# Kernel tuning notes

Hardware: AMD Instinct MI355X
Metric: run time of the kernel (lower is better)

The kernel has to match this reference:

```python
import jax, jax.numpy as jnp
import numpy as np

TOPOLOGY = [0,0,1,2,3,4,0,6,7,8,0,10,11,12,12,14,15,16,12,18,19,20]
J = len(TOPOLOGY)          # 22 joints
POS, OFF = 3, 1            # position_feature, offset_feature
CIN = (POS + OFF) * J      # 88 conv channels


def _adj():
    # adj[parent, child] = 1 (root skipped), fixed skeleton adjacency
    a = np.zeros((J, J), np.float32)
    for i, p in enumerate(TOPOLOGY):
        if i:
            a[p, i] = 1.0
    return jnp.asarray(a)


def setup_inputs() -> dict:
    key = jax.random.key(0)
    ks = jax.random.split(key, 32)

    def n(k, shape, s):
        return jax.random.normal(k, shape, dtype=jnp.float32) * s

    inp = {
        "input": jax.random.normal(ks[0], (128, 2048, J, POS), dtype=jnp.float32),
        "offset": jax.random.normal(ks[1], (128, 2048, J, OFF), dtype=jnp.float32),
    }
    i = 2
    for c in ("conv1", "conv2", "conv3"):
        inp[c + "_w"] = n(ks[i], (CIN, CIN, 4), 0.05); i += 1  # OIH
        inp[c + "_b"] = jnp.zeros((CIN,), jnp.float32)
    for g in ("g1", "g2"):
        inp[g + "_n2n_w"] = n(ks[i], (POS, POS), 0.3); i += 1
        inp[g + "_n2n_b"] = jnp.zeros((POS,), jnp.float32)
        inp[g + "_e2n_we"] = n(ks[i], (OFF, POS), 0.3); i += 1
        inp[g + "_e2n_wn"] = n(ks[i], (POS, POS), 0.3); i += 1
        inp[g + "_e2n_b"] = jnp.zeros((POS,), jnp.float32)
        inp[g + "_n2e_wn"] = n(ks[i], (POS, OFF), 0.3); i += 1
        inp[g + "_n2e_we"] = n(ks[i], (OFF, OFF), 0.3); i += 1
        inp[g + "_n2e_b"] = jnp.zeros((OFF,), jnp.float32)
        inp[g + "_lin_w"] = n(ks[i], (2 * POS, POS), 0.3); i += 1
        inp[g + "_lin_b"] = jnp.zeros((POS,), jnp.float32)
    return inp


def _conv_block(x, off, w, b):
    # concat node+edge feats, fold (joint, feature) into channels, temporal Conv1d k=4 s=2 p=1
    x = jnp.concatenate([x, off], axis=-1)          # [B,F,J,C]
    B, F, Jn, C = x.shape
    y = x.transpose(0, 2, 3, 1).reshape(B, Jn * C, F)
    y = jax.lax.conv_general_dilated(y, w, window_strides=(2,), padding=[(1, 1)],
                                     dimension_numbers=("NCH", "OIH", "NCH"))
    y = y + b[None, :, None]
    Fn = y.shape[-1]                                # F // 2
    return y.transpose(0, 2, 1).reshape(B, Fn, Jn, C)


def _graph_block(x, A, n2n_w, n2n_b, e2n_we, e2n_wn, e2n_b,
                 n2e_wn, n2e_we, n2e_b, lin_w, lin_b):
    node, edge = x[..., :POS], x[..., POS:]
    # adjacency broadcast (torch code replicated it B*F times; same math)
    agg_n = jnp.einsum('ij,bfjc->bfic', A, node)
    agg_e = jnp.einsum('ij,bfjc->bfic', A, edge)
    f1 = agg_n @ n2n_w + n2n_b                              # Node2Node
    f2 = agg_e @ e2n_we + node @ e2n_wn + e2n_b             # Edge2Node
    new_edge = jnp.einsum('ji,bfjc->bfic', A, node) @ n2e_wn + edge @ n2e_we + n2e_b  # Node2Edge
    h = jnp.concatenate([f1, f2], axis=-1) @ lin_w + lin_b  # fuse 2*c_out_node -> c_out_node
    return h, new_edge


def reference(input, offset,
              conv1_w, conv1_b, conv2_w, conv2_b, conv3_w, conv3_b,
              g1_n2n_w, g1_n2n_b, g1_e2n_we, g1_e2n_wn, g1_e2n_b,
              g1_n2e_wn, g1_n2e_we, g1_n2e_b, g1_lin_w, g1_lin_b,
              g2_n2n_w, g2_n2n_b, g2_e2n_we, g2_e2n_wn, g2_e2n_b,
              g2_n2e_wn, g2_n2e_we, g2_n2e_b, g2_lin_w, g2_lin_b):
    A = _adj()
    x = _conv_block(input, offset, conv1_w, conv1_b)
    x, off = _graph_block(x, A, g1_n2n_w, g1_n2n_b, g1_e2n_we, g1_e2n_wn, g1_e2n_b,
                          g1_n2e_wn, g1_n2e_we, g1_n2e_b, g1_lin_w, g1_lin_b)
    x = _conv_block(x, off, conv2_w, conv2_b)
    x, off = _graph_block(x, A, g2_n2n_w, g2_n2n_b, g2_e2n_we, g2_e2n_wn, g2_e2n_b,
                          g2_n2e_wn, g2_n2e_we, g2_n2e_b, g2_lin_w, g2_lin_b)
    x = _conv_block(x, off, conv3_w, conv3_b)
    return x[..., :POS]   # final slice when last dim != c_out_node
```

## Files before the change

kernel.cpp:

```cpp
#include <hip/hip_runtime.h>


static constexpr int Jn   = 22;
static constexpr int C4   = 88;
static constexpr int KK   = 352;
static constexpr int NPAD = 96;
static constexpr int LROW = 88;
static constexpr int YROW = 101;
static constexpr int WSWZ = 2 * 11 * 3 * 64 * 8;

typedef __attribute__((ext_vector_type(8))) short    short8;
typedef __attribute__((ext_vector_type(4))) float    floatx4;
typedef __attribute__((ext_vector_type(4))) unsigned uintx4;

__device__ constexpr int TOPc[Jn] = {0,0,1,2,3,4,0,6,7,8,0,10,11,12,12,14,15,16,12,18,19,20};

__device__ __forceinline__ unsigned short f2bf(float f) {
    unsigned u = __builtin_bit_cast(unsigned, f);
    unsigned r = (u + 0x7FFFu + ((u >> 16) & 1u)) >> 16;
    return (unsigned short)r;
}
__device__ __forceinline__ int qmap(int q) {
    return (q < 66) ? 4 * (q / 3) + (q % 3) : 4 * (q - 66) + 3;
}

struct GW {
    const float *n2n_w, *n2n_b, *e2n_we, *e2n_wn, *e2n_b;
    const float *n2e_wn, *n2e_we, *n2e_b, *lin_w, *lin_b;
};

__global__ __launch_bounds__(256)
void prep_weights(const float* __restrict__ w1, const float* __restrict__ w2,
                  const float* __restrict__ w3,
                  const float* __restrict__ b1, const float* __restrict__ b2,
                  const float* __restrict__ b3,
                  unsigned short* __restrict__ wo, float* __restrict__ bo)
{
    const int i = blockIdx.x * 256 + threadIdx.x;
    if (i < 3 * WSWZ) {
        const int s = i / WSWZ, e = i - s * WSWZ;
        const int j = e & 7, t = e >> 3;
        const int lane = t & 63, t2 = t >> 6;
        const int nti = t2 % 3, t3 = t2 / 3;
        const int kt = t3 % 11, nh = t3 / 11;
        const int co = nh * 48 + nti * 16 + (lane & 15);
        const int k  = kt * 32 + 8 * (lane >> 4) + j;
        const int tap = k / C4, q = k - tap * C4;
        const float* w = (s == 0) ? w1 : (s == 1) ? w2 : w3;
        float v = 0.f;
        if (co < C4) v = w[((size_t)qmap(co) * C4 + qmap(q)) * 4 + tap];
        wo[i] = f2bf(v);
    } else if (i < 3 * WSWZ + 3 * NPAD) {
        const int jj = i - 3 * WSWZ;
        const int s = jj / NPAD, q = jj - s * NPAD;
        const float* bb = (s == 0) ? b1 : (s == 1) ? b2 : b3;
        bo[jj] = (q < C4) ? bb[qmap(q)] : 0.f;
    }
}

template<int FIN, int INM, int OUTM, int MTt>
__global__ __launch_bounds__(256, (MTt == 128 ? 2 : 4))
void conv_fused(const float* __restrict__ xf, const float* __restrict__ xoff,
                const unsigned short* __restrict__ xbf,
                const unsigned short* __restrict__ bwz, const float* __restrict__ bias,
                void* __restrict__ yout, GW g)
{
    constexpr int FOUT  = FIN / 2;
    constexpr int NTILE = FOUT / MTt;
    constexpr int NFRt  = 2 * MTt + 2;
    constexpr int NMT   = MTt / 32;
    constexpr int CHK_N  = NFRt * 11;
    constexpr int NIT_C  = (CHK_N + 255) / 256;
    constexpr int NGRP   = 256 / MTt;
    constexpr int JPG    = (Jn + NGRP - 1) / NGRP;
    constexpr unsigned XBYTES = NFRt * LROW * 2;
    constexpr unsigned SMEM = (OUTM == 0)
        ? (MTt * YROW * 4 + MTt * C4 * 2)
        : (XBYTES + MTt * 66 * 4);

    __shared__ __align__(16) unsigned char smem[SMEM];
    unsigned short* Xs = reinterpret_cast<unsigned short*>(smem);
    float*          Yt = reinterpret_cast<float*>(smem);
    unsigned short* OutU = reinterpret_cast<unsigned short*>(smem + (size_t)MTt * YROW * 4);
    float*          OutF = reinterpret_cast<float*>(smem + XBYTES);

    const int tid = threadIdx.x;
    const int b   = blockIdx.x / NTILE;
    const int fo0 = (blockIdx.x - b * NTILE) * MTt;
    const int gf0 = 2 * fo0 - 1;

    if (INM == 0) {
        const float* nbase = xf   + (size_t)b * FIN * 66;
        const float* ebase = xoff + (size_t)b * FIN * 22;
#pragma unroll
        for (int it = 0; it < NIT_C; ++it) {
            const int idx = tid + it * 256;
            if (idx < CHK_N) {
                const int lf = idx / 11, qq = idx - lf * 11;
                const int gf = gf0 + lf;
                const int gfc = min(max(gf, 0), FIN - 1);
                const float* nrow = nbase + (size_t)gfc * 66;
                const float* erow = ebase + (size_t)gfc * 22;
                uintx4 u;
#pragma unroll
                for (int k = 0; k < 4; ++k) {
                    const int gq = qq * 8 + 2 * k;
                    const float* src = (gq >= 66) ? (erow + (gq - 66)) : (nrow + gq);
                    const float2 v = *reinterpret_cast<const float2*>(src);
                    u[k] = (unsigned)f2bf(v.x) | ((unsigned)f2bf(v.y) << 16);
                }
                if (gf != gfc) u = (uintx4){0u, 0u, 0u, 0u};
                *reinterpret_cast<uintx4*>(Xs + lf * LROW + qq * 8) = u;
            }
        }
    } else {
        const uintx4* xsrc = reinterpret_cast<const uintx4*>(xbf) + (size_t)b * FIN * 11;
#pragma unroll
        for (int it = 0; it < NIT_C; ++it) {
            const int idx = tid + it * 256;
            if (idx < CHK_N) {
                const int lf = idx / 11, qq = idx - lf * 11;
                const int gf = gf0 + lf;
                const int gfc = min(max(gf, 0), FIN - 1);
                uintx4 v = xsrc[gfc * 11 + qq];
                if (gf != gfc) v = (uintx4){0u, 0u, 0u, 0u};
                *reinterpret_cast<uintx4*>(Xs + lf * LROW + qq * 8) = v;
            }
        }
    }
    __syncthreads();

    const int wid = tid >> 6, lane = tid & 63;
    const int l15 = lane & 15, h = lane >> 4;
    const int mhalf = wid >> 1, nhalf = wid & 1;

    floatx4 acc[NMT][3];
#pragma unroll
    for (int mt = 0; mt < NMT; ++mt)
#pragma unroll
        for (int nti = 0; nti < 3; ++nti)
            acc[mt][nti] = (floatx4){0.f, 0.f, 0.f, 0.f};

    const unsigned short* wb = bwz + ((size_t)nhalf * 33 * 64 + lane) * 8;

#pragma unroll
    for (int kt = 0; kt < 11; ++kt) {
        const int q   = 4 * kt + h;
        const int tap = (unsigned)q / 11u;
        const int ci0 = 8 * (q - 11 * tap);
        const int lfb = 2 * l15 + tap;

        short8 afr[NMT];
#pragma unroll
        for (int mt = 0; mt < NMT; ++mt)
            afr[mt] = *reinterpret_cast<const short8*>(
                Xs + (mhalf * MTt + mt * 32 + lfb) * LROW + ci0);

        short8 bfr[3];
#pragma unroll
        for (int nti = 0; nti < 3; ++nti)
            bfr[nti] = *reinterpret_cast<const short8*>(wb + (size_t)(kt * 3 + nti) * 64 * 8);

#pragma unroll
        for (int mt = 0; mt < NMT; ++mt)
#pragma unroll
            for (int nti = 0; nti < 3; ++nti)
                acc[mt][nti] = __builtin_amdgcn_mfma_f32_16x16x32_bf16(
                    afr[mt], bfr[nti], acc[mt][nti], 0, 0, 0);
    }

    if (OUTM == 1) {
#pragma unroll
        for (int mt = 0; mt < NMT; ++mt)
#pragma unroll
            for (int nti = 0; nti < 3; ++nti) {
                const int co = nhalf * 48 + nti * 16 + l15;
                if (co < 66) {
                    const float bi = bias[co];
#pragma unroll
                    for (int r = 0; r < 4; ++r) {
                        const int row = mhalf * (MTt / 2) + mt * 16 + 4 * h + r;
                        OutF[row * 66 + co] = acc[mt][nti][r] + bi;
                    }
                }
            }
        __syncthreads();
        float2* dstg = reinterpret_cast<float2*>(
            reinterpret_cast<float*>(yout) + (size_t)(b * FOUT + fo0) * 66);
        const float2* srcl = reinterpret_cast<const float2*>(OutF);
        constexpr int NOUT2 = MTt * 33;
#pragma unroll
        for (int it = 0; it < (NOUT2 + 255) / 256; ++it) {
            const int idx = tid + it * 256;
            if (idx < NOUT2) dstg[idx] = srcl[idx];
        }
        return;
    }

    __syncthreads();
#pragma unroll
    for (int mt = 0; mt < NMT; ++mt)
#pragma unroll
        for (int nti = 0; nti < 3; ++nti) {
            const int co = nhalf * 48 + nti * 16 + l15;
            const float bi = bias[co];
#pragma unroll
            for (int r = 0; r < 4; ++r) {
                const int row = mhalf * (MTt / 2) + mt * 16 + 4 * h + r;
                Yt[row * YROW + co] = acc[mt][nti][r] + bi;
            }
        }
    __syncthreads();

    {
        const int row = tid & (MTt - 1), grp = tid / MTt;
        const float* yr = Yt + row * YROW;

        float n2n[9], n2nb[3], e2we[3], e2wn[9], e2nb[3], newn[3], lin[18], linb[3];
#pragma unroll
        for (int i = 0; i < 9;  ++i) n2n[i]  = g.n2n_w[i];
#pragma unroll
        for (int i = 0; i < 3;  ++i) n2nb[i] = g.n2n_b[i];
#pragma unroll
        for (int i = 0; i < 3;  ++i) e2we[i] = g.e2n_we[i];
#pragma unroll
        for (int i = 0; i < 9;  ++i) e2wn[i] = g.e2n_wn[i];
#pragma unroll
        for (int i = 0; i < 3;  ++i) e2nb[i] = g.e2n_b[i];
#pragma unroll
        for (int i = 0; i < 3;  ++i) newn[i] = g.n2e_wn[i];
        const float newe = g.n2e_we[0];
        const float neb  = g.n2e_b[0];
#pragma unroll
        for (int i = 0; i < 18; ++i) lin[i]  = g.lin_w[i];
#pragma unroll
        for (int i = 0; i < 3;  ++i) linb[i] = g.lin_b[i];

#pragma unroll
        for (int i = 0; i < Jn; ++i) {
            if (i / JPG != grp) continue;
            float an0 = 0.f, an1 = 0.f, an2 = 0.f, ae = 0.f;
#pragma unroll
            for (int j = 1; j < Jn; ++j) {
                if (TOPc[j] == i) {
                    an0 += yr[3 * j]; an1 += yr[3 * j + 1];
                    an2 += yr[3 * j + 2]; ae += yr[66 + j];
                }
            }
            const float s0 = yr[3 * i], s1 = yr[3 * i + 1], s2 = yr[3 * i + 2], se = yr[66 + i];
            float f1[3], f2[3];
#pragma unroll
            for (int c = 0; c < 3; ++c) {
                f1[c] = an0 * n2n[c] + an1 * n2n[3 + c] + an2 * n2n[6 + c] + n2nb[c];
                f2[c] = ae * e2we[c] + s0 * e2wn[c] + s1 * e2wn[3 + c] + s2 * e2wn[6 + c] + e2nb[c];
            }
            float p0 = 0.f, p1 = 0.f, p2 = 0.f;
            if (i > 0) {
                const int p = TOPc[i];
                p0 = yr[3 * p]; p1 = yr[3 * p + 1]; p2 = yr[3 * p + 2];
            }
            const float ne = p0 * newn[0] + p1 * newn[1] + p2 * newn[2] + se * newe + neb;

            float o[3];
#pragma unroll
            for (int c = 0; c < 3; ++c)
                o[c] = f1[0] * lin[0 + c] + f1[1] * lin[3 + c] + f1[2] * lin[6 + c]
                     + f2[0] * lin[9 + c] + f2[1] * lin[12 + c] + f2[2] * lin[15 + c] + linb[c];

            OutU[row * C4 + 3 * i]     = f2bf(o[0]);
            OutU[row * C4 + 3 * i + 1] = f2bf(o[1]);
            OutU[row * C4 + 3 * i + 2] = f2bf(o[2]);
            OutU[row * C4 + 66 + i]    = f2bf(ne);
        }
    }
    __syncthreads();

    {
        uintx4* dstg = reinterpret_cast<uintx4*>(
            reinterpret_cast<unsigned short*>(yout) + (size_t)(b * FOUT + fo0) * C4);
        const uintx4* srcl = reinterpret_cast<const uintx4*>(OutU);
        constexpr int NOUT = MTt * 11;
#pragma unroll
        for (int it = 0; it < (NOUT + 255) / 256; ++it) {
            const int idx = tid + it * 256;
            if (idx < NOUT) dstg[idx] = srcl[idx];
        }
    }
}

extern "C" void kernel_launch(void* const* d_in, const int* in_sizes, int n_in,
                              void* d_out, int out_size, void* d_ws, size_t ws_size,
                              hipStream_t stream)
{
    (void)n_in; (void)out_size; (void)ws_size;

    const float* input  = (const float*)d_in[0];
    const float* offset = (const float*)d_in[1];
    const float* c1w = (const float*)d_in[2]; const float* c1b = (const float*)d_in[3];
    const float* c2w = (const float*)d_in[4]; const float* c2b = (const float*)d_in[5];
    const float* c3w = (const float*)d_in[6]; const float* c3b = (const float*)d_in[7];

    GW g1 { (const float*)d_in[8],  (const float*)d_in[9],  (const float*)d_in[10],
            (const float*)d_in[11], (const float*)d_in[12], (const float*)d_in[13],
            (const float*)d_in[14], (const float*)d_in[15], (const float*)d_in[16],
            (const float*)d_in[17] };
    GW g2 { (const float*)d_in[18], (const float*)d_in[19], (const float*)d_in[20],
            (const float*)d_in[21], (const float*)d_in[22], (const float*)d_in[23],
            (const float*)d_in[24], (const float*)d_in[25], (const float*)d_in[26],
            (const float*)d_in[27] };

    const int B = in_sizes[0] / (2048 * Jn * 3);

    unsigned short* wbf = (unsigned short*)d_ws;
    float* pb = (float*)(wbf + (size_t)3 * WSWZ);
    unsigned short* X1 = (unsigned short*)(pb + 3 * NPAD);
    unsigned short* X2 = X1 + (size_t)B * 1024 * C4;

    {
        const int tot = 3 * WSWZ + 3 * NPAD;
        prep_weights<<<(tot + 255) / 256, 256, 0, stream>>>(c1w, c2w, c3w, c1b, c2b, c3b, wbf, pb);
    }

    conv_fused<2048, 0, 0, 128><<<B * 8, 256, 0, stream>>>(input, offset, nullptr,
                                                           wbf, pb, X1, g1);
    conv_fused<1024, 1, 0, 128><<<B * 4, 256, 0, stream>>>(nullptr, nullptr, X1,
                                                           wbf + WSWZ, pb + NPAD, X2, g2);
    conv_fused<512, 1, 1, 64><<<B * 4, 256, 0, stream>>>(nullptr, nullptr, X2,
                                                         wbf + 2 * WSWZ, pb + 2 * NPAD, d_out, g2);
}
```

Baseline: 68.18 us.

## Roll loops, prefetch B fragments, and use packed child tables in graph epilogue

Replaces the fully unrolled K loop with a rolled loop that software-prefetches the next step's weight fragments into registers. Reduces unrolling across the load, epilogue and store loops to cut code size and register pressure. The graph epilogue swaps the unrolled 22-joint scan with predicated skips for a rolled per-thread loop that looks up children and parent in bit-packed 5-bit tables. The rolled loops may lose instruction-level parallelism and add runtime indexing of shared memory.

```diff
diff --git a/kernel.cpp b/kernel.cpp
--- a/kernel.cpp
+++ b/kernel.cpp
@@ -14,6 +14,31 @@
 typedef __attribute__((ext_vector_type(4))) unsigned uintx4;
 
 __device__ constexpr int TOPc[Jn] = {0,0,1,2,3,4,0,6,7,8,0,10,11,12,12,14,15,16,12,18,19,20};
+
+constexpr int CH0v[22] = {1,2,3,4,5,31,7,8,9,31,11,12,13,31,15,16,17,31,19,20,21,31};
+constexpr int CH1v[22] = {6,31,31,31,31,31,31,31,31,31,31,31,14,31,31,31,31,31,31,31,31,31};
+constexpr int CH2v[22] = {10,31,31,31,31,31,31,31,31,31,31,31,18,31,31,31,31,31,31,31,31,31};
+constexpr int PARv[22] = {0,0,1,2,3,4,0,6,7,8,0,10,11,12,12,14,15,16,12,18,19,20};
+constexpr unsigned long long pklo(const int* v) {
+    unsigned long long r = 0;
+    for (int k = 0; k < 12; ++k) r |= (unsigned long long)(v[k] & 31) << (5 * k);
+    return r;
+}
+constexpr unsigned long long pkhi(const int* v) {
+    unsigned long long r = 0;
+    for (int k = 12; k < 22; ++k) r |= (unsigned long long)(v[k] & 31) << (5 * (k - 12));
+    return r;
+}
+constexpr unsigned long long CH0_LO = pklo(CH0v), CH0_HI = pkhi(CH0v);
+constexpr unsigned long long CH1_LO = pklo(CH1v), CH1_HI = pkhi(CH1v);
+constexpr unsigned long long CH2_LO = pklo(CH2v), CH2_HI = pkhi(CH2v);
+constexpr unsigned long long PAR_LO = pklo(PARv), PAR_HI = pkhi(PARv);
+
+__device__ __forceinline__ int tbl5(unsigned long long lo, unsigned long long hi, int i) {
+    const unsigned long long w = (i < 12) ? lo : hi;
+    const int sh = (i < 12) ? 5 * i : 5 * (i - 12);
+    return (int)((w >> sh) & 31);
+}
 
 __device__ __forceinline__ unsigned short f2bf(float f) {
     unsigned u = __builtin_bit_cast(unsigned, f);
@@ -92,7 +117,7 @@
     if (INM == 0) {
         const float* nbase = xf   + (size_t)b * FIN * 66;
         const float* ebase = xoff + (size_t)b * FIN * 22;
-#pragma unroll
+#pragma unroll 2
         for (int it = 0; it < NIT_C; ++it) {
             const int idx = tid + it * 256;
             if (idx < CHK_N) {
@@ -115,7 +140,7 @@
         }
     } else {
         const uintx4* xsrc = reinterpret_cast<const uintx4*>(xbf) + (size_t)b * FIN * 11;
-#pragma unroll
+#pragma unroll 2
         for (int it = 0; it < NIT_C; ++it) {
             const int idx = tid + it * 256;
             if (idx < CHK_N) {
@@ -143,8 +168,19 @@
 
     const unsigned short* wb = bwz + ((size_t)nhalf * 33 * 64 + lane) * 8;
 
-#pragma unroll
+    short8 bcur[3];
+#pragma unroll
+    for (int nti = 0; nti < 3; ++nti)
+        bcur[nti] = *reinterpret_cast<const short8*>(wb + (size_t)nti * 512);
+
+#pragma unroll 1
     for (int kt = 0; kt < 11; ++kt) {
+        const int ktn = min(kt + 1, 10);
+        short8 bnxt[3];
+#pragma unroll
+        for (int nti = 0; nti < 3; ++nti)
+            bnxt[nti] = *reinterpret_cast<const short8*>(wb + (size_t)(ktn * 3 + nti) * 512);
+
         const int q   = 4 * kt + h;
         const int tap = (unsigned)q / 11u;
         const int ci0 = 8 * (q - 11 * tap);
@@ -156,21 +192,19 @@
             afr[mt] = *reinterpret_cast<const short8*>(
                 Xs + (mhalf * MTt + mt * 32 + lfb) * LROW + ci0);
 
-        short8 bfr[3];
-#pragma unroll
-        for (int nti = 0; nti < 3; ++nti)
-            bfr[nti] = *reinterpret_cast<const short8*>(wb + (size_t)(kt * 3 + nti) * 64 * 8);
-
 #pragma unroll
         for (int mt = 0; mt < NMT; ++mt)
 #pragma unroll
             for (int nti = 0; nti < 3; ++nti)
                 acc[mt][nti] = __builtin_amdgcn_mfma_f32_16x16x32_bf16(
-                    afr[mt], bfr[nti], acc[mt][nti], 0, 0, 0);
+                    afr[mt], bcur[nti], acc[mt][nti], 0, 0, 0);
+
+#pragma unroll
+        for (int nti = 0; nti < 3; ++nti) bcur[nti] = bnxt[nti];
     }
 
     if (OUTM == 1) {
-#pragma unroll
+#pragma unroll 1
         for (int mt = 0; mt < NMT; ++mt)
 #pragma unroll
             for (int nti = 0; nti < 3; ++nti) {
@@ -189,7 +223,7 @@
             reinterpret_cast<float*>(yout) + (size_t)(b * FOUT + fo0) * 66);
         const float2* srcl = reinterpret_cast<const float2*>(OutF);
         constexpr int NOUT2 = MTt * 33;
-#pragma unroll
+#pragma unroll 1
         for (int it = 0; it < (NOUT2 + 255) / 256; ++it) {
             const int idx = tid + it * 256;
             if (idx < NOUT2) dstg[idx] = srcl[idx];
@@ -198,7 +232,7 @@
     }
 
     __syncthreads();
-#pragma unroll
+#pragma unroll 1
     for (int mt = 0; mt < NMT; ++mt)
 #pragma unroll
         for (int nti = 0; nti < 3; ++nti) {
@@ -236,41 +270,43 @@
 #pragma unroll
         for (int i = 0; i < 3;  ++i) linb[i] = g.lin_b[i];
 
-#pragma unroll
-        for (int i = 0; i < Jn; ++i) {
-            if (i / JPG != grp) continue;
-            float an0 = 0.f, an1 = 0.f, an2 = 0.f, ae = 0.f;
-#pragma unroll
-            for (int j = 1; j < Jn; ++j) {
-                if (TOPc[j] == i) {
-                    an0 += yr[3 * j]; an1 += yr[3 * j + 1];
-                    an2 += yr[3 * j + 2]; ae += yr[66 + j];
+        unsigned short* outr = OutU + row * C4;
+
+#pragma unroll 1
+        for (int ii = 0; ii < JPG; ++ii) {
+            const int i = grp * JPG + ii;
+            if (i < Jn) {
+                float an0 = 0.f, an1 = 0.f, an2 = 0.f, ae = 0.f;
+                int c = tbl5(CH0_LO, CH0_HI, i);
+                if (c != 31) { an0 += yr[3*c]; an1 += yr[3*c+1]; an2 += yr[3*c+2]; ae += yr[66+c]; }
+                c = tbl5(CH1_LO, CH1_HI, i);
+                if (c != 31) { an0 += yr[3*c]; an1 += yr[3*c+1]; an2 += yr[3*c+2]; ae += yr[66+c]; }
+                c = tbl5(CH2_LO, CH2_HI, i);
+                if (c != 31) { an0 += yr[3*c]; an1 += yr[3*c+1]; an2 += yr[3*c+2]; ae += yr[66+c]; }
+
+                const float s0 = yr[3*i], s1 = yr[3*i+1], s2 = yr[3*i+2], se = yr[66+i];
+                float f1[3], f2[3];
+#pragma unroll
+                for (int cc = 0; cc < 3; ++cc) {
+                    f1[cc] = an0 * n2n[cc] + an1 * n2n[3+cc] + an2 * n2n[6+cc] + n2nb[cc];
+                    f2[cc] = ae * e2we[cc] + s0 * e2wn[cc] + s1 * e2wn[3+cc] + s2 * e2wn[6+cc] + e2nb[cc];
                 }
-            }
-            const float s0 = yr[3 * i], s1 = yr[3 * i + 1], s2 = yr[3 * i + 2], se = yr[66 + i];
-            float f1[3], f2[3];
-#pragma unroll
-            for (int c = 0; c < 3; ++c) {
-                f1[c] = an0 * n2n[c] + an1 * n2n[3 + c] + an2 * n2n[6 + c] + n2nb[c];
-                f2[c] = ae * e2we[c] + s0 * e2wn[c] + s1 * e2wn[3 + c] + s2 * e2wn[6 + c] + e2nb[c];
-            }
-            float p0 = 0.f, p1 = 0.f, p2 = 0.f;
-            if (i > 0) {
-                const int p = TOPc[i];
-                p0 = yr[3 * p]; p1 = yr[3 * p + 1]; p2 = yr[3 * p + 2];
-            }
-            const float ne = p0 * newn[0] + p1 * newn[1] + p2 * newn[2] + se * newe + neb;
-
-            float o[3];
-#pragma unroll
-            for (int c = 0; c < 3; ++c)
-                o[c] = f1[0] * lin[0 + c] + f1[1] * lin[3 + c] + f1[2] * lin[6 + c]
-                     + f2[0] * lin[9 + c] + f2[1] * lin[12 + c] + f2[2] * lin[15 + c] + linb[c];
-
-            OutU[row * C4 + 3 * i]     = f2bf(o[0]);
-            OutU[row * C4 + 3 * i + 1] = f2bf(o[1]);
-            OutU[row * C4 + 3 * i + 2] = f2bf(o[2]);
-            OutU[row * C4 + 66 + i]    = f2bf(ne);
+                const int p = tbl5(PAR_LO, PAR_HI, i);
+                float p0 = 0.f, p1 = 0.f, p2 = 0.f;
+                if (i > 0) { p0 = yr[3*p]; p1 = yr[3*p+1]; p2 = yr[3*p+2]; }
+                const float ne = p0 * newn[0] + p1 * newn[1] + p2 * newn[2] + se * newe + neb;
+
+                float o[3];
+#pragma unroll
+                for (int cc = 0; cc < 3; ++cc)
+                    o[cc] = f1[0] * lin[0+cc] + f1[1] * lin[3+cc] + f1[2] * lin[6+cc]
+                          + f2[0] * lin[9+cc] + f2[1] * lin[12+cc] + f2[2] * lin[15+cc] + linb[cc];
+
+                outr[3*i]     = f2bf(o[0]);
+                outr[3*i + 1] = f2bf(o[1]);
+                outr[3*i + 2] = f2bf(o[2]);
+                outr[66 + i]  = f2bf(ne);
+            }
         }
     }
     __syncthreads();
@@ -280,7 +316,7 @@
             reinterpret_cast<unsigned short*>(yout) + (size_t)(b * FOUT + fo0) * C4);
         const uintx4* srcl = reinterpret_cast<const uintx4*>(OutU);
         constexpr int NOUT = MTt * 11;
-#pragma unroll
+#pragma unroll 1
         for (int it = 0; it < (NOUT + 255) / 256; ++it) {
             const int idx = tid + it * 256;
             if (idx < NOUT) dstg[idx] = srcl[idx];
```

New measurement: 98.01 us. 43.8% more time.

## Process graph epilogue in two row halves to shrink LDS and raise occupancy

Applied to the files above, without the earlier changes.

The graph-block epilogue of the fused conv kernel now handles the M tile in two 64-row halves. Each half stages accumulators into a reused LDS buffer, computes the graph ops with four thread groups of six joints each, and writes out before the next half. This drops the epilogue LDS footprint to fit within the input staging buffer, and the launch bound for 128-row tiles is raised from 2 to 3 blocks per SM. The cost is extra barriers and a serialized epilogue, plus the risk of register spills under the tighter launch bound. The hardcoded 64-row halves assume MTt is 128.

```diff
diff --git a/kernel.cpp b/kernel.cpp
--- a/kernel.cpp
+++ b/kernel.cpp
@@ -59,7 +59,7 @@
 }
 
 template<int FIN, int INM, int OUTM, int MTt>
-__global__ __launch_bounds__(256, (MTt == 128 ? 2 : 4))
+__global__ __launch_bounds__(256, (MTt == 128 ? 3 : 4))
 void conv_fused(const float* __restrict__ xf, const float* __restrict__ xoff,
                 const unsigned short* __restrict__ xbf,
                 const unsigned short* __restrict__ bwz, const float* __restrict__ bias,
@@ -71,17 +71,13 @@
     constexpr int NMT   = MTt / 32;
     constexpr int CHK_N  = NFRt * 11;
     constexpr int NIT_C  = (CHK_N + 255) / 256;
-    constexpr int NGRP   = 256 / MTt;
-    constexpr int JPG    = (Jn + NGRP - 1) / NGRP;
     constexpr unsigned XBYTES = NFRt * LROW * 2;
-    constexpr unsigned SMEM = (OUTM == 0)
-        ? (MTt * YROW * 4 + MTt * C4 * 2)
-        : (XBYTES + MTt * 66 * 4);
+    constexpr unsigned SMEM = (OUTM == 0) ? XBYTES : (XBYTES + MTt * 66 * 4);
 
     __shared__ __align__(16) unsigned char smem[SMEM];
     unsigned short* Xs = reinterpret_cast<unsigned short*>(smem);
     float*          Yt = reinterpret_cast<float*>(smem);
-    unsigned short* OutU = reinterpret_cast<unsigned short*>(smem + (size_t)MTt * YROW * 4);
+    unsigned short* OutU = reinterpret_cast<unsigned short*>(smem + 64 * YROW * 4);
     float*          OutF = reinterpret_cast<float*>(smem + XBYTES);
 
     const int tid = threadIdx.x;
@@ -197,94 +193,102 @@
         return;
     }
 
+    float n2n[9], n2nb[3], e2we[3], e2wn[9], e2nb[3], newn[3], lin[18], linb[3];
+#pragma unroll
+    for (int i = 0; i < 9;  ++i) n2n[i]  = g.n2n_w[i];
+#pragma unroll
+    for (int i = 0; i < 3;  ++i) n2nb[i] = g.n2n_b[i];
+#pragma unroll
+    for (int i = 0; i < 3;  ++i) e2we[i] = g.e2n_we[i];
+#pragma unroll
+    for (int i = 0; i < 9;  ++i) e2wn[i] = g.e2n_wn[i];
+#pragma unroll
+    for (int i = 0; i < 3;  ++i) e2nb[i] = g.e2n_b[i];
+#pragma unroll
+    for (int i = 0; i < 3;  ++i) newn[i] = g.n2e_wn[i];
+    const float newe = g.n2e_we[0];
+    const float neb  = g.n2e_b[0];
+#pragma unroll
+    for (int i = 0; i < 18; ++i) lin[i]  = g.lin_w[i];
+#pragma unroll
+    for (int i = 0; i < 3;  ++i) linb[i] = g.lin_b[i];
+
     __syncthreads();
-#pragma unroll
-    for (int mt = 0; mt < NMT; ++mt)
-#pragma unroll
-        for (int nti = 0; nti < 3; ++nti) {
-            const int co = nhalf * 48 + nti * 16 + l15;
-            const float bi = bias[co];
-#pragma unroll
-            for (int r = 0; r < 4; ++r) {
-                const int row = mhalf * (MTt / 2) + mt * 16 + 4 * h + r;
-                Yt[row * YROW + co] = acc[mt][nti][r] + bi;
-            }
-        }
-    __syncthreads();
-
-    {
-        const int row = tid & (MTt - 1), grp = tid / MTt;
-        const float* yr = Yt + row * YROW;
-
-        float n2n[9], n2nb[3], e2we[3], e2wn[9], e2nb[3], newn[3], lin[18], linb[3];
-#pragma unroll
-        for (int i = 0; i < 9;  ++i) n2n[i]  = g.n2n_w[i];
-#pragma unroll
-        for (int i = 0; i < 3;  ++i) n2nb[i] = g.n2n_b[i];
-#pragma unroll
-        for (int i = 0; i < 3;  ++i) e2we[i] = g.e2n_we[i];
-#pragma unroll
-        for (int i = 0; i < 9;  ++i) e2wn[i] = g.e2n_wn[i];
-#pragma unroll
-        for (int i = 0; i < 3;  ++i) e2nb[i] = g.e2n_b[i];
-#pragma unroll
-        for (int i = 0; i < 3;  ++i) newn[i] = g.n2e_wn[i];
-        const float newe = g.n2e_we[0];
-        const float neb  = g.n2e_b[0];
-#pragma unroll
-        for (int i = 0; i < 18; ++i) lin[i]  = g.lin_w[i];
-#pragma unroll
-        for (int i = 0; i < 3;  ++i) linb[i] = g.lin_b[i];
-
-#pragma unroll
-        for (int i = 0; i < Jn; ++i) {
-            if (i / JPG != grp) continue;
-            float an0 = 0.f, an1 = 0.f, an2 = 0.f, ae = 0.f;
-#pragma unroll
-            for (int j = 1; j < Jn; ++j) {
-                if (TOPc[j] == i) {
-                    an0 += yr[3 * j]; an1 += yr[3 * j + 1];
-                    an2 += yr[3 * j + 2]; ae += yr[66 + j];
-                }
-            }
-            const float s0 = yr[3 * i], s1 = yr[3 * i + 1], s2 = yr[3 * i + 2], se = yr[66 + i];
-            float f1[3], f2[3];
-#pragma unroll
-            for (int c = 0; c < 3; ++c) {
-                f1[c] = an0 * n2n[c] + an1 * n2n[3 + c] + an2 * n2n[6 + c] + n2nb[c];
-                f2[c] = ae * e2we[c] + s0 * e2wn[c] + s1 * e2wn[3 + c] + s2 * e2wn[6 + c] + e2nb[c];
-            }
-            float p0 = 0.f, p1 = 0.f, p2 = 0.f;
-            if (i > 0) {
-                const int p = TOPc[i];
-                p0 = yr[3 * p]; p1 = yr[3 * p + 1]; p2 = yr[3 * p + 2];
-            }
-            const float ne = p0 * newn[0] + p1 * newn[1] + p2 * newn[2] + se * newe + neb;
-
-            float o[3];
-#pragma unroll
-            for (int c = 0; c < 3; ++c)
-                o[c] = f1[0] * lin[0 + c] + f1[1] * lin[3 + c] + f1[2] * lin[6 + c]
-                     + f2[0] * lin[9 + c] + f2[1] * lin[12 + c] + f2[2] * lin[15 + c] + linb[c];
-
-            OutU[row * C4 + 3 * i]     = f2bf(o[0]);
-            OutU[row * C4 + 3 * i + 1] = f2bf(o[1]);
-            OutU[row * C4 + 3 * i + 2] = f2bf(o[2]);
-            OutU[row * C4 + 66 + i]    = f2bf(ne);
-        }
-    }
-    __syncthreads();
-
-    {
-        uintx4* dstg = reinterpret_cast<uintx4*>(
-            reinterpret_cast<unsigned short*>(yout) + (size_t)(b * FOUT + fo0) * C4);
-        const uintx4* srcl = reinterpret_cast<const uintx4*>(OutU);
-        constexpr int NOUT = MTt * 11;
-#pragma unroll
-        for (int it = 0; it < (NOUT + 255) / 256; ++it) {
-            const int idx = tid + it * 256;
-            if (idx < NOUT) dstg[idx] = srcl[idx];
-        }
+
+#pragma unroll
+    for (int half = 0; half < 2; ++half) {
+        if (mhalf == half) {
+#pragma unroll
+            for (int mt = 0; mt < NMT; ++mt)
+#pragma unroll
+                for (int nti = 0; nti < 3; ++nti) {
+                    const int co = nhalf * 48 + nti * 16 + l15;
+                    const float bi = bias[co];
+#pragma unroll
+                    for (int r = 0; r < 4; ++r) {
+                        const int row = mt * 16 + 4 * h + r;
+                        Yt[row * YROW + co] = acc[mt][nti][r] + bi;
+                    }
+                }
+        }
+        __syncthreads();
+
+        {
+            const int row = tid & 63, grp = tid >> 6;
+            const float* yr = Yt + row * YROW;
+            unsigned short* outr = OutU + row * C4;
+
+#pragma unroll
+            for (int i = 0; i < Jn; ++i) {
+                if (i / 6 != grp) continue;
+                float an0 = 0.f, an1 = 0.f, an2 = 0.f, ae = 0.f;
+#pragma unroll
+                for (int j = 1; j < Jn; ++j) {
+                    if (TOPc[j] == i) {
+                        an0 += yr[3 * j]; an1 += yr[3 * j + 1];
+                        an2 += yr[3 * j + 2]; ae += yr[66 + j];
+                    }
+                }
+                const float s0 = yr[3 * i], s1 = yr[3 * i + 1], s2 = yr[3 * i + 2], se = yr[66 + i];
+                float f1[3], f2[3];
+#pragma unroll
+                for (int c = 0; c < 3; ++c) {
+                    f1[c] = an0 * n2n[c] + an1 * n2n[3 + c] + an2 * n2n[6 + c] + n2nb[c];
+                    f2[c] = ae * e2we[c] + s0 * e2wn[c] + s1 * e2wn[3 + c] + s2 * e2wn[6 + c] + e2nb[c];
+                }
+                float p0 = 0.f, p1 = 0.f, p2 = 0.f;
+                if (i > 0) {
+                    const int p = TOPc[i];
+                    p0 = yr[3 * p]; p1 = yr[3 * p + 1]; p2 = yr[3 * p + 2];
+                }
+                const float ne = p0 * newn[0] + p1 * newn[1] + p2 * newn[2] + se * newe + neb;
+
+                float o[3];
+#pragma unroll
+                for (int c = 0; c < 3; ++c)
+                    o[c] = f1[0] * lin[0 + c] + f1[1] * lin[3 + c] + f1[2] * lin[6 + c]
+                         + f2[0] * lin[9 + c] + f2[1] * lin[12 + c] + f2[2] * lin[15 + c] + linb[c];
+
+                outr[3 * i]     = f2bf(o[0]);
+                outr[3 * i + 1] = f2bf(o[1]);
+                outr[3 * i + 2] = f2bf(o[2]);
+                outr[66 + i]    = f2bf(ne);
+            }
+        }
+        __syncthreads();
+
+        {
+            uintx4* dstg = reinterpret_cast<uintx4*>(
+                reinterpret_cast<unsigned short*>(yout)
+                + (size_t)(b * FOUT + fo0 + half * 64) * C4);
+            const uintx4* srcl = reinterpret_cast<const uintx4*>(OutU);
+#pragma unroll
+            for (int it = 0; it < 3; ++it) {
+                const int idx = tid + it * 256;
+                if (idx < 704) dstg[idx] = srcl[idx];
+            }
+        }
+        __syncthreads();
     }
 }
 
```

Result: no change. 68.91 us (+1.1%).
